# Optimization experiments

Hardware: AMD Instinct MI355X
Metric: run time of the kernel (lower is better)

The kernel has to match this reference:

```python
import jax, jax.numpy as jnp
import numpy as np

EPS = 1e-5

def _bn(x, g, b, axes):
    m = jnp.mean(x, axes, keepdims=True)
    v = jnp.var(x, axes, keepdims=True)
    return (x - m) * jax.lax.rsqrt(v + EPS) * g + b

def _fps(p, m):
    # farthest point sampling: p [B,N,3] -> int32 indices [B,m]
    B, N, _ = p.shape
    def step(carry, _):
        mind, last = carry
        lastp = jnp.take_along_axis(p, last[:, None, None], axis=1)[:, 0]  # [B,3]
        d = jnp.sum((p - lastp[:, None, :]) ** 2, axis=-1)                 # [B,N]
        mind = jnp.minimum(mind, d)
        nxt = jnp.argmax(mind, axis=1).astype(jnp.int32)
        return (mind, nxt), last
    init = (jnp.full((B, N), jnp.inf, p.dtype), jnp.zeros((B,), jnp.int32))
    _, idxs = jax.lax.scan(step, init, None, length=m)  # [m,B]
    return idxs.T

def _gather(x, idx):
    # x [B,N,C], idx [B,...] -> [B,...,C]
    B, C = x.shape[0], x.shape[-1]
    flat = idx.reshape(B, -1)
    out = jnp.take_along_axis(x, flat[:, :, None], axis=1)
    return out.reshape(idx.shape + (C,))

def _transition_down(p, h, W, g, b, stride, nsample):
    # p [B,N,3], h [B,N,C] -> new_p [B,N//stride,3], y [B,N//stride,Cout]
    B, N, _ = p.shape
    M = N // stride
    idx = _fps(p, M)
    new_p = _gather(p, idx)                                               # [B,M,3]
    d = jnp.sum((new_p[:, :, None, :] - p[:, None, :, :]) ** 2, axis=-1)  # [B,M,N]
    _, nidx = jax.lax.top_k(-d, nsample)                                  # [B,M,k]
    gp = _gather(p, nidx) - new_p[:, :, None, :]                          # rel xyz [B,M,k,3]
    gx = _gather(h, nidx)                                                 # [B,M,k,C]
    feat = jnp.concatenate([gp, gx], axis=-1)                             # with_xyz=True
    y = jnp.einsum('bmkc,cd->bmkd', feat, W)
    y = jax.nn.relu(_bn(y, g, b, (0, 1, 2)))
    return new_p, jnp.max(y, axis=2)                                      # MaxPool1d(nsample)

def _forward(x, W1, g1, b1, W2, g2, b2, W3, g3, b3, W4, g4, b4, W5, g5, b5,
             Wc1, bc1, gc1, hc1, Wc2, bc2, gc2, hc2, Wc3, bc3):
    p = x[..., :3]                                    # in_channels == 3 -> features = xyz
    h = jnp.einsum('bnc,cd->bnd', p, W1)
    h = jax.nn.relu(_bn(h, g1, b1, (0, 1)))           # enc1: stride=1
    p, h = _transition_down(p, h, W2, g2, b2, 4, 16)  # enc2
    p, h = _transition_down(p, h, W3, g3, b3, 4, 16)  # enc3
    p, h = _transition_down(p, h, W4, g4, b4, 4, 16)  # enc4
    p, h = _transition_down(p, h, W5, g5, b5, 4, 16)  # enc5
    z = jnp.mean(h, axis=1)                           # segment-mean pool -> [B,512]
    z = jax.nn.relu(_bn(z @ Wc1 + bc1, gc1, hc1, (0,)))   # Dropout = identity (eval)
    z = jax.nn.relu(_bn(z @ Wc2 + bc2, gc2, hc2, (0,)))
    return z @ Wc3 + bc3                              # [B,40]

def setup_inputs() -> dict:
    key = jax.random.key(0)
    ks = jax.random.split(key, 16)
    B, N = 16, 4096
    def lin(k, fi, fo):
        return (jax.random.normal(k, (fi, fo), jnp.float32) / np.sqrt(fi)).astype(jnp.float32)
    inp = {"x": jax.random.normal(ks[0], (B, N, 3), jnp.float32)}
    planes = [32, 64, 128, 256, 512]
    ins = [3, 3 + 32, 3 + 64, 3 + 128, 3 + 256]
    for i, (fi, fo) in enumerate(zip(ins, planes), start=1):
        inp[f"W{i}"] = lin(ks[i], fi, fo)
        inp[f"g{i}"] = jnp.ones((fo,), jnp.float32)
        inp[f"b{i}"] = jnp.zeros((fo,), jnp.float32)
    dims = [(512, 256), (256, 128), (128, 40)]
    for j, (fi, fo) in enumerate(dims, start=1):
        inp[f"Wc{j}"] = lin(ks[5 + j], fi, fo)
        inp[f"bc{j}"] = jnp.zeros((fo,), jnp.float32)
        if j < 3:
            inp[f"gc{j}"] = jnp.ones((fo,), jnp.float32)
            inp[f"hc{j}"] = jnp.zeros((fo,), jnp.float32)
    return inp

def reference(x, W1, g1, b1, W2, g2, b2, W3, g3, b3, W4, g4, b4, W5, g5, b5,
              Wc1, bc1, gc1, hc1, Wc2, bc2, gc2, hc2, Wc3, bc3):
    return _forward(x, W1, g1, b1, W2, g2, b2, W3, g3, b3, W4, g4, b4, W5, g5, b5,
                    Wc1, bc1, gc1, hc1, Wc2, bc2, gc2, hc2, Wc3, bc3)
```

## Files before the change

kernel.cpp:

```cpp
#include <hip/hip_runtime.h>
#include <math.h>
#include <float.h>

#define BN_EPS 1e-5f

__device__ __forceinline__ float sqdist_exact(float dx, float dy, float dz) {
  return __fadd_rn(__fadd_rn(__fmul_rn(dx, dx), __fmul_rn(dy, dy)), __fmul_rn(dz, dz));
}

__global__ void __launch_bounds__(256) mlp1_kernel(const float* __restrict__ x,
                                                   const float* __restrict__ W1,
                                                   float* __restrict__ h1, int rows) {
  int tid = blockIdx.x * 256 + threadIdx.x;
  int row = tid >> 5;
  int d = tid & 31;
  if (row >= rows) return;
  float x0 = x[row * 3 + 0], x1 = x[row * 3 + 1], x2 = x[row * 3 + 2];
  float acc = x0 * W1[d] + x1 * W1[32 + d] + x2 * W1[64 + d];
  h1[row * 32 + d] = acc;
}

__global__ void stats_kernel(const float* __restrict__ v, int n, int D,
                             float* __restrict__ partial) {
  int tid = blockIdx.x * blockDim.x + threadIdx.x;
  int stride = blockDim.x * gridDim.x;
  float s = 0.f, q = 0.f;
  for (int i = tid; i < n; i += stride) { float a = v[i]; s += a; q += a * a; }
  int c = tid % D;
  extern __shared__ float sm[];
  for (int i = threadIdx.x; i < 2 * D; i += blockDim.x) sm[i] = 0.f;
  __syncthreads();
  atomicAdd(&sm[c], s);
  atomicAdd(&sm[D + c], q);
  __syncthreads();
  for (int i = threadIdx.x; i < 2 * D; i += blockDim.x)
    atomicAdd(&partial[(blockIdx.x & 63) * 2 * D + i], sm[i]);
}

__global__ void finalize_kernel(const float* __restrict__ partial,
                                const float* __restrict__ g, const float* __restrict__ b,
                                float cnt, int D, float* __restrict__ ss) {
  int d = threadIdx.x;
  if (d >= D) return;
  float s = 0.f, q = 0.f;
  for (int j = 0; j < 64; j++) { s += partial[j * 2 * D + d]; q += partial[j * 2 * D + D + d]; }
  float mean = s / cnt;
  float var = q / cnt - mean * mean;
  var = fmaxf(var, 0.f);
  float sc = g[d] * rsqrtf(var + BN_EPS);
  ss[d] = sc;
  ss[D + d] = b[d] - mean * sc;
}

__global__ void bn_apply_kernel(float* __restrict__ vmax, const float* __restrict__ vmin,
                                const float* __restrict__ ss, int D, int n) {
  int tid = blockIdx.x * blockDim.x + threadIdx.x;
  int stride = blockDim.x * gridDim.x;
  for (int i = tid; i < n; i += stride) {
    int d = i % D;
    float sc = ss[d], sh = ss[D + d];
    float v = (sc >= 0.f) ? vmax[i] : vmin[i];
    vmax[i] = fmaxf(v * sc + sh, 0.f);
  }
}

#define DPP_STEP(CTRL)                                                                   \
  {                                                                                      \
    unsigned int nhi = (unsigned int)__builtin_amdgcn_update_dpp((int)khi, (int)khi,     \
                                                                 CTRL, 0xf, 0xf, false); \
    unsigned int nlo = (unsigned int)__builtin_amdgcn_update_dpp((int)klo, (int)klo,     \
                                                                 CTRL, 0xf, 0xf, false); \
    unsigned long long nk = (((unsigned long long)nhi) << 32) | nlo;                     \
    if (nk > wk) { wk = nk; khi = nhi; klo = nlo; }                                      \
  }

template <int P, int NW>
__device__ __forceinline__ void fps_body(const float* __restrict__ pb,
                                         float* __restrict__ newp_b,
                                         float* spts, float* snew,
                                         unsigned long long* slots, int t) {
  constexpr int BS = NW * 64;
  constexpr int N = P * BS;
  constexpr int M = N / 4;
  const int wv = t >> 6;
  const int lane = t & 63;
  float px[P], py[P], pz[P], md[P];
#pragma unroll
  for (int j = 0; j < P; j++) {
    int i = j * BS + t;
    float x = pb[3 * i], y = pb[3 * i + 1], z = pb[3 * i + 2];
    px[j] = x; py[j] = y; pz[j] = z; md[j] = INFINITY;
    spts[3 * i] = x; spts[3 * i + 1] = y; spts[3 * i + 2] = z;
  }
  float lx = pb[0], ly = pb[1], lz = pb[2];
  if (t == 0) {
    if constexpr (NW > 1) {
      snew[0] = lx; snew[1] = ly; snew[2] = lz;
    } else {
      newp_b[0] = lx; newp_b[1] = ly; newp_b[2] = lz;
    }
  }

  for (int r = 1; r < M; r++) {
    float bv; int bi;
    {
      float d0 = sqdist_exact(px[0] - lx, py[0] - ly, pz[0] - lz);
      float m0 = fminf(md[0], d0);
      md[0] = m0;
      bv = m0; bi = t;
    }
#pragma unroll
    for (int j = 1; j < P; j++) {
      float d = sqdist_exact(px[j] - lx, py[j] - ly, pz[j] - lz);
      float m = fminf(md[j], d);
      md[j] = m;
      if (m > bv) { bv = m; bi = j * BS + t; }
    }
    unsigned int khi = __float_as_uint(bv);
    unsigned int klo = ~(unsigned int)bi;
    unsigned long long wk = (((unsigned long long)khi) << 32) | klo;
    DPP_STEP(0x111);
    DPP_STEP(0x112);
    DPP_STEP(0x114);
    DPP_STEP(0x118);
    DPP_STEP(0x142);
    DPP_STEP(0x143);
    unsigned int gidx;
    if constexpr (NW == 1) {
      unsigned int wlo = (unsigned int)__builtin_amdgcn_readlane((int)wk, 63);
      gidx = ~wlo;
    } else {
      unsigned long long* base = slots + (r & 1) * NW;
      if (lane == 63) base[wv] = wk;
      __syncthreads();
      unsigned long long fk = base[0];
#pragma unroll
      for (int w = 1; w < NW; w++) {
        unsigned long long k2 = base[w];
        if (k2 > fk) fk = k2;
      }
      gidx = ~(unsigned int)fk;
    }
    lx = spts[3 * gidx];
    ly = spts[3 * gidx + 1];
    lz = spts[3 * gidx + 2];
    if (t == 0) {
      if constexpr (NW > 1) {
        snew[3 * r] = lx; snew[3 * r + 1] = ly; snew[3 * r + 2] = lz;
      } else {
        newp_b[3 * r] = lx; newp_b[3 * r + 1] = ly; newp_b[3 * r + 2] = lz;
      }
    }
  }
  if constexpr (NW > 1) {
    __syncthreads();
    for (int i = t; i < M * 3; i += BS) newp_b[i] = snew[i];
  }
}

template <int P, int NW>
__global__ void __launch_bounds__(NW * 64) fps4_kernel(const float* __restrict__ p,
                                                       float* __restrict__ newp) {
  constexpr int BS = NW * 64;
  constexpr int N = P * BS;
  constexpr int M = N / 4;
  __shared__ float spts[N * 3];
  __shared__ float snew[NW > 1 ? M * 3 : 1];
  __shared__ unsigned long long slots[NW > 1 ? 2 * NW : 2];
  fps_body<P, NW>(p + (size_t)blockIdx.x * N * 3, newp + (size_t)blockIdx.x * M * 3,
                  spts, snew, slots, threadIdx.x);
}

__device__ __forceinline__ void knn_body(const float* __restrict__ p,
                                         const float* __restrict__ newp,
                                         int N, int M, int BM,
                                         int* __restrict__ nidx,
                                         int gwid, int lane) {
  if (gwid >= BM) return;
  int b = gwid / M;
  const float* pb = p + (size_t)b * N * 3;
  float qx = newp[(size_t)gwid * 3], qy = newp[(size_t)gwid * 3 + 1], qz = newp[(size_t)gwid * 3 + 2];
  float bd[16];
  int bi[16];
#pragma unroll
  for (int s = 0; s < 16; s++) { bd[s] = INFINITY; bi[s] = 0x7FFFFFFF; }
  for (int c = lane; c < N; c += 64) {
    float d = sqdist_exact(pb[3 * c] - qx, pb[3 * c + 1] - qy, pb[3 * c + 2] - qz);
    if (d < bd[15]) {
      bd[15] = d; bi[15] = c;
#pragma unroll
      for (int s = 15; s >= 1; --s) {
        bool sw = bd[s] < bd[s - 1];
        if (sw) {
          float tf = bd[s]; bd[s] = bd[s - 1]; bd[s - 1] = tf;
          int ti = bi[s]; bi[s] = bi[s - 1]; bi[s - 1] = ti;
        }
      }
    }
  }
  int out = 0;
  for (int r = 0; r < 16; r++) {
    float v = bd[0]; int ii = bi[0];
    float mv = v; int mi = ii;
#pragma unroll
    for (int m = 1; m < 64; m <<= 1) {
      float v2 = __shfl_xor(mv, m);
      int i2 = __shfl_xor(mi, m);
      if (v2 < mv || (v2 == mv && i2 < mi)) { mv = v2; mi = i2; }
    }
    if (mi == ii) {
#pragma unroll
      for (int s = 0; s < 15; s++) { bd[s] = bd[s + 1]; bi[s] = bi[s + 1]; }
      bd[15] = INFINITY; bi[15] = 0x7FFFFFFF;
    }
    if (lane == r) out = mi;
  }
  if (lane < 16) nidx[(size_t)gwid * 16 + lane] = out;
}

__device__ __forceinline__ void gemm_body(
    float* sm, const float* __restrict__ p, const float* __restrict__ h,
    const float* __restrict__ newp, const int* __restrict__ nidx,
    const float* __restrict__ W, float* __restrict__ ymax, float* __restrict__ ymin,
    float* __restrict__ partial, int N, int M, int BM, int Ch, int Cpad, int D,
    int Gseq, int bid, int t) {
  int Ctot = Ch + 3;
  int TD = D < 256 ? D : 256;
  int Gpar = 256 / TD;
  float* sfeat = sm;
  float* sstat = sm + Gpar * 16 * Cpad;
  for (int i = t; i < 2 * D; i += 256) sstat[i] = 0.f;
  int mloc = t / TD;
  int dbase = t % TD;
  int DV = D / TD;
  __syncthreads();
  for (int s = 0; s < Gseq; s++) {
    int grp0 = (bid * Gseq + s) * Gpar;
    if (grp0 >= BM) break;
    int nf = Gpar * 16 * Cpad;
    for (int i = t; i < nf; i += 256) {
      int c = i % Cpad;
      int rk = i / Cpad;
      int k = rk & 15;
      int g = rk >> 4;
      int grp = grp0 + g;
      float val = 0.f;
      if (grp < BM && c < Ctot) {
        int b = grp / M;
        int nb = nidx[(size_t)grp * 16 + k];
        if (c < 3)
          val = p[((size_t)b * N + nb) * 3 + c] - newp[(size_t)grp * 3 + c];
        else
          val = h[((size_t)b * N + nb) * Ch + (c - 3)];
      }
      sfeat[i] = val;
    }
    __syncthreads();
    int grp = grp0 + mloc;
    bool act = grp < BM;
    const float* fr = sfeat + mloc * 16 * Cpad;
    for (int dv = 0; dv < DV; ++dv) {
      int d = dbase + (dv << 8);
      float acc[16];
#pragma unroll
      for (int k = 0; k < 16; k++) acc[k] = 0.f;
      for (int c = 0; c < Cpad; c += 4) {
        float w0 = (c < Ctot) ? W[(size_t)c * D + d] : 0.f;
        float w1 = (c + 1 < Ctot) ? W[(size_t)(c + 1) * D + d] : 0.f;
        float w2 = (c + 2 < Ctot) ? W[(size_t)(c + 2) * D + d] : 0.f;
        float w3 = (c + 3 < Ctot) ? W[(size_t)(c + 3) * D + d] : 0.f;
#pragma unroll
        for (int k = 0; k < 16; k++) {
          const float4 f = *reinterpret_cast<const float4*>(fr + k * Cpad + c);
          acc[k] += f.x * w0 + f.y * w1 + f.z * w2 + f.w * w3;
        }
      }
      if (act) {
        float ssum = 0.f, ssq = 0.f, amax = -INFINITY, amin = INFINITY;
#pragma unroll
        for (int k = 0; k < 16; k++) {
          float a = acc[k];
          ssum += a; ssq += a * a;
          amax = fmaxf(amax, a); amin = fminf(amin, a);
        }
        ymax[(size_t)grp * D + d] = amax;
        ymin[(size_t)grp * D + d] = amin;
        atomicAdd(&sstat[d], ssum);
        atomicAdd(&sstat[D + d], ssq);
      }
    }
    __syncthreads();
  }
  for (int i = t; i < 2 * D; i += 256)
    atomicAdd(&partial[(bid & 63) * 2 * D + i], sstat[i]);
}

template <int P, int NW>
__global__ void __launch_bounds__(256) fused_fps_knn_kernel(
    const float* __restrict__ fp, float* __restrict__ fnewp,
    const float* __restrict__ kp, const float* __restrict__ knewp,
    int kN, int kM, int kBM, int* __restrict__ knidx) {
  constexpr int BS = NW * 64;
  constexpr int N = P * BS;
  constexpr int M = N / 4;
  __shared__ float spts[N * 3];
  __shared__ float snew[NW > 1 ? M * 3 : 1];
  __shared__ unsigned long long slots[NW > 1 ? 2 * NW : 2];
  const int t = threadIdx.x;
  if (blockIdx.x < 16) {
    if (NW > 1 || t < 64) {
      fps_body<P, NW>(fp + (size_t)blockIdx.x * N * 3, fnewp + (size_t)blockIdx.x * M * 3,
                      spts, snew, slots, t);
    }
  } else {
    int gwid = ((blockIdx.x - 16) * 256 + t) >> 6;
    int lane = t & 63;
    knn_body(kp, knewp, kN, kM, kBM, knidx, gwid, lane);
  }
}

template <int P, int NW>
__global__ void __launch_bounds__(256) fused_gfk_kernel(
    const float* __restrict__ p, const float* __restrict__ h,
    const float* __restrict__ newp, const int* __restrict__ nidx,
    const float* __restrict__ W, float* __restrict__ ymax, float* __restrict__ ymin,
    float* __restrict__ partial, int N, int M, int BM, int Ch, int Cpad, int D,
    int Gseq, int nGemm,
    const float* __restrict__ fp, float* __restrict__ fnewp, int nFps,
    const float* __restrict__ kp, const float* __restrict__ knewp,
    int kN, int kM, int kBM, int* __restrict__ knidx) {
  constexpr int FBS = NW * 64;
  constexpr int FN = P * FBS;
  constexpr int FM = FN / 4;
  __shared__ float spts[FN * 3];
  __shared__ float snew[NW > 1 ? FM * 3 : 1];
  __shared__ unsigned long long slots[NW > 1 ? 2 * NW : 2];
  extern __shared__ float sm[];
  const int t = threadIdx.x;
  const int bid = blockIdx.x;
  if (bid < nGemm) {
    gemm_body(sm, p, h, newp, nidx, W, ymax, ymin, partial,
              N, M, BM, Ch, Cpad, D, Gseq, bid, t);
  } else if (bid < nGemm + nFps) {
    int fb = bid - nGemm;
    if (NW > 1 || t < 64) {
      fps_body<P, NW>(fp + (size_t)fb * FN * 3, fnewp + (size_t)fb * FM * 3,
                      spts, snew, slots, t);
    }
  } else {
    int gwid = ((bid - nGemm - nFps) * 256 + t) >> 6;
    knn_body(kp, knewp, kN, kM, kBM, knidx, gwid, t & 63);
  }
}

__global__ void __launch_bounds__(256) gemm_kernel(
    const float* __restrict__ p, const float* __restrict__ h, const float* __restrict__ newp,
    const int* __restrict__ nidx, const float* __restrict__ W,
    float* __restrict__ ymax, float* __restrict__ ymin, float* __restrict__ partial,
    int N, int M, int BM, int Ch, int Cpad, int D, int Gseq) {
  extern __shared__ float sm[];
  gemm_body(sm, p, h, newp, nidx, W, ymax, ymin, partial,
            N, M, BM, Ch, Cpad, D, Gseq, blockIdx.x, threadIdx.x);
}

__global__ void __launch_bounds__(512) classifier_kernel(
    const float* __restrict__ h4,
    const float* __restrict__ Wc1, const float* __restrict__ bc1,
    const float* __restrict__ gc1, const float* __restrict__ hc1,
    const float* __restrict__ Wc2, const float* __restrict__ bc2,
    const float* __restrict__ gc2, const float* __restrict__ hc2,
    const float* __restrict__ Wc3, const float* __restrict__ bc3,
    float* __restrict__ out) {
  __shared__ float z[16 * 512];
  __shared__ float z1[16 * 256];
  __shared__ float z2[16 * 128];
  __shared__ float sc[256], sh[256];
  int t = threadIdx.x;
  for (int i = t; i < 16 * 512; i += 512) {
    int b = i >> 9, c = i & 511;
    float s = 0.f;
    for (int k = 0; k < 16; k++) s += h4[((size_t)b * 16 + k) * 512 + c];
    z[i] = s * (1.f / 16.f);
  }
  __syncthreads();
  for (int i = t; i < 16 * 256; i += 512) {
    int b = i >> 8, d = i & 255;
    float a = bc1[d];
    for (int c = 0; c < 512; c++) a += z[(b << 9) + c] * Wc1[c * 256 + d];
    z1[i] = a;
  }
  __syncthreads();
  if (t < 256) {
    float s = 0.f, q = 0.f;
    for (int b = 0; b < 16; b++) { float a = z1[(b << 8) + t]; s += a; q += a * a; }
    float mean = s * (1.f / 16.f);
    float var = fmaxf(q * (1.f / 16.f) - mean * mean, 0.f);
    float scl = gc1[t] * rsqrtf(var + BN_EPS);
    sc[t] = scl; sh[t] = hc1[t] - mean * scl;
  }
  __syncthreads();
  for (int i = t; i < 16 * 256; i += 512) {
    int d = i & 255;
    z1[i] = fmaxf(z1[i] * sc[d] + sh[d], 0.f);
  }
  __syncthreads();
  for (int i = t; i < 16 * 128; i += 512) {
    int b = i >> 7, d = i & 127;
    float a = bc2[d];
    for (int c = 0; c < 256; c++) a += z1[(b << 8) + c] * Wc2[c * 128 + d];
    z2[i] = a;
  }
  __syncthreads();
  if (t < 128) {
    float s = 0.f, q = 0.f;
    for (int b = 0; b < 16; b++) { float a = z2[(b << 7) + t]; s += a; q += a * a; }
    float mean = s * (1.f / 16.f);
    float var = fmaxf(q * (1.f / 16.f) - mean * mean, 0.f);
    float scl = gc2[t] * rsqrtf(var + BN_EPS);
    sc[t] = scl; sh[t] = hc2[t] - mean * scl;
  }
  __syncthreads();
  for (int i = t; i < 16 * 128; i += 512) {
    int d = i & 127;
    z2[i] = fmaxf(z2[i] * sc[d] + sh[d], 0.f);
  }
  __syncthreads();
  for (int i = t; i < 640; i += 512) {
    int b = i / 40, d = i % 40;
    float a = bc3[d];
    for (int c = 0; c < 128; c++) a += z2[(b << 7) + c] * Wc3[c * 40 + d];
    out[i] = a;
  }
}

extern "C" void kernel_launch(void* const* d_in, const int* in_sizes, int n_in,
                              void* d_out, int out_size, void* d_ws, size_t ws_size,
                              hipStream_t stream) {
  (void)in_sizes; (void)n_in; (void)out_size; (void)ws_size;
  const float* x   = (const float*)d_in[0];
  const float* W1  = (const float*)d_in[1];
  const float* g1  = (const float*)d_in[2];
  const float* b1  = (const float*)d_in[3];
  const float* W2  = (const float*)d_in[4];
  const float* g2  = (const float*)d_in[5];
  const float* b2  = (const float*)d_in[6];
  const float* W3  = (const float*)d_in[7];
  const float* g3  = (const float*)d_in[8];
  const float* b3  = (const float*)d_in[9];
  const float* W4  = (const float*)d_in[10];
  const float* g4  = (const float*)d_in[11];
  const float* b4  = (const float*)d_in[12];
  const float* W5  = (const float*)d_in[13];
  const float* g5  = (const float*)d_in[14];
  const float* b5  = (const float*)d_in[15];
  const float* Wc1 = (const float*)d_in[16];
  const float* bc1 = (const float*)d_in[17];
  const float* gc1 = (const float*)d_in[18];
  const float* hc1 = (const float*)d_in[19];
  const float* Wc2 = (const float*)d_in[20];
  const float* bc2 = (const float*)d_in[21];
  const float* gc2 = (const float*)d_in[22];
  const float* hc2 = (const float*)d_in[23];
  const float* Wc3 = (const float*)d_in[24];
  const float* bc3 = (const float*)d_in[25];
  float* out = (float*)d_out;

  float* ws = (float*)d_ws;
  float* HA    = ws;
  float* HB    = HA + 2097152;
  float* YMIN  = HB + 1048576;
  float* NP1   = YMIN + 1048576;
  float* NP2   = NP1 + 49152;
  float* NP3   = NP2 + 12288;
  float* NP4   = NP3 + 3072;
  int*   NIDX1 = (int*)(NP4 + 768);
  int*   NIDX2 = NIDX1 + 262144;
  int*   NIDX3 = NIDX2 + 65536;
  int*   NIDX4 = NIDX3 + 16384;
  float* PART  = (float*)(NIDX4 + 4096);
  float* SS    = PART + 5 * 65536;

  hipMemsetAsync(PART, 0, 5 * 65536 * sizeof(float), stream);

  mlp1_kernel<<<(65536 * 32) / 256, 256, 0, stream>>>(x, W1, HA, 65536);
  stats_kernel<<<256, 256, 2 * 32 * sizeof(float), stream>>>(HA, 65536 * 32, 32, PART);
  finalize_kernel<<<1, 32, 0, stream>>>(PART, g1, b1, 65536.f, 32, SS);
  bn_apply_kernel<<<512, 256, 0, stream>>>(HA, HA, SS, 32, 65536 * 32);

  fps4_kernel<16, 4><<<16, 256, 0, stream>>>(x, NP1);
  fused_fps_knn_kernel<4, 4><<<16 + 4096, 256, 0, stream>>>(
      NP1, NP2, x, NP1, 4096, 1024, 16384, NIDX1);

  fused_gfk_kernel<4, 1><<<512 + 16 + 1024, 256, (4 * 16 * 36 + 2 * 64) * sizeof(float), stream>>>(
      x, HA, NP1, NIDX1, W2, HB, YMIN, PART + 65536, 4096, 1024, 16384, 32, 36, 64, 8, 512,
      NP2, NP3, 16,
      NP1, NP2, 1024, 256, 4096, NIDX2);
  finalize_kernel<<<1, 64, 0, stream>>>(PART + 65536, g2, b2, (float)(16384 * 16), 64, SS + 1024);
  bn_apply_kernel<<<512, 256, 0, stream>>>(HB, YMIN, SS + 1024, 64, 16384 * 64);

  fused_gfk_kernel<1, 1><<<512 + 16 + 256, 256, (2 * 16 * 68 + 2 * 128) * sizeof(float), stream>>>(
      NP1, HB, NP2, NIDX2, W3, HA, YMIN, PART + 2 * 65536, 1024, 256, 4096, 64, 68, 128, 4, 512,
      NP3, NP4, 16,
      NP2, NP3, 256, 64, 1024, NIDX3);
  finalize_kernel<<<1, 128, 0, stream>>>(PART + 2 * 65536, g3, b3, (float)(4096 * 16), 128, SS + 2048);
  bn_apply_kernel<<<512, 256, 0, stream>>>(HA, YMIN, SS + 2048, 128, 4096 * 128);

  fused_gfk_kernel<1, 1><<<512 + 0 + 64, 256, (16 * 132 + 2 * 256) * sizeof(float), stream>>>(
      NP2, HA, NP3, NIDX3, W4, HB, YMIN, PART + 3 * 65536, 256, 64, 1024, 128, 132, 256, 2, 512,
      nullptr, nullptr, 0,
      NP3, NP4, 64, 16, 256, NIDX4);
  finalize_kernel<<<1, 256, 0, stream>>>(PART + 3 * 65536, g4, b4, (float)(1024 * 16), 256, SS + 3072);
  bn_apply_kernel<<<512, 256, 0, stream>>>(HB, YMIN, SS + 3072, 256, 1024 * 256);

  gemm_kernel<<<256, 256, (16 * 260 + 2 * 512) * sizeof(float), stream>>>(
      NP3, HB, NP4, NIDX4, W5, HA, YMIN, PART + 4 * 65536, 64, 16, 256, 256, 260, 512, 1);
  finalize_kernel<<<1, 512, 0, stream>>>(PART + 4 * 65536, g5, b5, (float)(256 * 16), 512, SS + 4096);
  bn_apply_kernel<<<512, 256, 0, stream>>>(HA, YMIN, SS + 4096, 512, 256 * 512);

  classifier_kernel<<<1, 512, 0, stream>>>(HA, Wc1, bc1, gc1, hc1, Wc2, bc2, gc2, hc2, Wc3, bc3, out);
}
```

Baseline: 1.378 ms.

## Merge launches: fuse FPS with MLP1, stats into FPS/KNN, finalize into BN apply

Runs the first farthest-point sampling in the same launch as the layer-1 pointwise MLP, and moves the layer-1 BN statistics into the combined FPS/KNN launch as extra blocks. Each finalize+bn_apply pair becomes a single kernel in which every block recomputes the scale and shift from the partial sums. This cuts roughly a dozen small launches and lets the cheap work overlap the serial FPS blocks. In exchange, each of the 512 blocks repeats the 64-way partial reduction.

```diff
diff --git a/kernel.cpp b/kernel.cpp
--- a/kernel.cpp
+++ b/kernel.cpp
@@ -6,62 +6,6 @@
 
 __device__ __forceinline__ float sqdist_exact(float dx, float dy, float dz) {
   return __fadd_rn(__fadd_rn(__fmul_rn(dx, dx), __fmul_rn(dy, dy)), __fmul_rn(dz, dz));
-}
-
-__global__ void __launch_bounds__(256) mlp1_kernel(const float* __restrict__ x,
-                                                   const float* __restrict__ W1,
-                                                   float* __restrict__ h1, int rows) {
-  int tid = blockIdx.x * 256 + threadIdx.x;
-  int row = tid >> 5;
-  int d = tid & 31;
-  if (row >= rows) return;
-  float x0 = x[row * 3 + 0], x1 = x[row * 3 + 1], x2 = x[row * 3 + 2];
-  float acc = x0 * W1[d] + x1 * W1[32 + d] + x2 * W1[64 + d];
-  h1[row * 32 + d] = acc;
-}
-
-__global__ void stats_kernel(const float* __restrict__ v, int n, int D,
-                             float* __restrict__ partial) {
-  int tid = blockIdx.x * blockDim.x + threadIdx.x;
-  int stride = blockDim.x * gridDim.x;
-  float s = 0.f, q = 0.f;
-  for (int i = tid; i < n; i += stride) { float a = v[i]; s += a; q += a * a; }
-  int c = tid % D;
-  extern __shared__ float sm[];
-  for (int i = threadIdx.x; i < 2 * D; i += blockDim.x) sm[i] = 0.f;
-  __syncthreads();
-  atomicAdd(&sm[c], s);
-  atomicAdd(&sm[D + c], q);
-  __syncthreads();
-  for (int i = threadIdx.x; i < 2 * D; i += blockDim.x)
-    atomicAdd(&partial[(blockIdx.x & 63) * 2 * D + i], sm[i]);
-}
-
-__global__ void finalize_kernel(const float* __restrict__ partial,
-                                const float* __restrict__ g, const float* __restrict__ b,
-                                float cnt, int D, float* __restrict__ ss) {
-  int d = threadIdx.x;
-  if (d >= D) return;
-  float s = 0.f, q = 0.f;
-  for (int j = 0; j < 64; j++) { s += partial[j * 2 * D + d]; q += partial[j * 2 * D + D + d]; }
-  float mean = s / cnt;
-  float var = q / cnt - mean * mean;
-  var = fmaxf(var, 0.f);
-  float sc = g[d] * rsqrtf(var + BN_EPS);
-  ss[d] = sc;
-  ss[D + d] = b[d] - mean * sc;
-}
-
-__global__ void bn_apply_kernel(float* __restrict__ vmax, const float* __restrict__ vmin,
-                                const float* __restrict__ ss, int D, int n) {
-  int tid = blockIdx.x * blockDim.x + threadIdx.x;
-  int stride = blockDim.x * gridDim.x;
-  for (int i = tid; i < n; i += stride) {
-    int d = i % D;
-    float sc = ss[d], sh = ss[D + d];
-    float v = (sc >= 0.f) ? vmax[i] : vmin[i];
-    vmax[i] = fmaxf(v * sc + sh, 0.f);
-  }
 }
 
 #define DPP_STEP(CTRL)                                                                   \
@@ -158,19 +102,6 @@
   }
 }
 
-template <int P, int NW>
-__global__ void __launch_bounds__(NW * 64) fps4_kernel(const float* __restrict__ p,
-                                                       float* __restrict__ newp) {
-  constexpr int BS = NW * 64;
-  constexpr int N = P * BS;
-  constexpr int M = N / 4;
-  __shared__ float spts[N * 3];
-  __shared__ float snew[NW > 1 ? M * 3 : 1];
-  __shared__ unsigned long long slots[NW > 1 ? 2 * NW : 2];
-  fps_body<P, NW>(p + (size_t)blockIdx.x * N * 3, newp + (size_t)blockIdx.x * M * 3,
-                  spts, snew, slots, threadIdx.x);
-}
-
 __device__ __forceinline__ void knn_body(const float* __restrict__ p,
                                          const float* __restrict__ newp,
                                          int N, int M, int BM,
@@ -216,6 +147,23 @@
     if (lane == r) out = mi;
   }
   if (lane < 16) nidx[(size_t)gwid * 16 + lane] = out;
+}
+
+__device__ __forceinline__ void stats_body(const float* __restrict__ v, int n, int D,
+                                           float* __restrict__ partial, float* sm,
+                                           int bid, int nb, int t) {
+  int tid = bid * 256 + t;
+  int stride = 256 * nb;
+  float s = 0.f, q = 0.f;
+  for (int i = tid; i < n; i += stride) { float a = v[i]; s += a; q += a * a; }
+  int c = tid % D;
+  for (int i = t; i < 2 * D; i += 256) sm[i] = 0.f;
+  __syncthreads();
+  atomicAdd(&sm[c], s);
+  atomicAdd(&sm[D + c], q);
+  __syncthreads();
+  for (int i = t; i < 2 * D; i += 256)
+    atomicAdd(&partial[(bid & 63) * 2 * D + i], sm[i]);
 }
 
 __device__ __forceinline__ void gemm_body(
@@ -295,27 +243,46 @@
     atomicAdd(&partial[(bid & 63) * 2 * D + i], sstat[i]);
 }
 
-template <int P, int NW>
-__global__ void __launch_bounds__(256) fused_fps_knn_kernel(
+__global__ void __launch_bounds__(256) fused_fps1_mlp1_kernel(
+    const float* __restrict__ x, float* __restrict__ newp,
+    const float* __restrict__ W1, float* __restrict__ h1, int rows) {
+  __shared__ float spts[4096 * 3];
+  __shared__ float snew[1024 * 3];
+  __shared__ unsigned long long slots[8];
+  const int t = threadIdx.x;
+  if (blockIdx.x < 16) {
+    fps_body<16, 4>(x + (size_t)blockIdx.x * 4096 * 3, newp + (size_t)blockIdx.x * 1024 * 3,
+                    spts, snew, slots, t);
+  } else {
+    int tid = (blockIdx.x - 16) * 256 + t;
+    int row = tid >> 5;
+    int d = tid & 31;
+    if (row < rows) {
+      float x0 = x[row * 3 + 0], x1 = x[row * 3 + 1], x2 = x[row * 3 + 2];
+      h1[row * 32 + d] = x0 * W1[d] + x1 * W1[32 + d] + x2 * W1[64 + d];
+    }
+  }
+}
+
+__global__ void __launch_bounds__(256) fused_fks_kernel(
     const float* __restrict__ fp, float* __restrict__ fnewp,
     const float* __restrict__ kp, const float* __restrict__ knewp,
-    int kN, int kM, int kBM, int* __restrict__ knidx) {
-  constexpr int BS = NW * 64;
-  constexpr int N = P * BS;
-  constexpr int M = N / 4;
-  __shared__ float spts[N * 3];
-  __shared__ float snew[NW > 1 ? M * 3 : 1];
-  __shared__ unsigned long long slots[NW > 1 ? 2 * NW : 2];
+    int kN, int kM, int kBM, int* __restrict__ knidx, int nKnn,
+    const float* __restrict__ sv, int sn, int sD, float* __restrict__ spartial, int nStats) {
+  __shared__ float spts[1024 * 3];
+  __shared__ float snew[256 * 3];
+  __shared__ unsigned long long slots[8];
+  __shared__ float ssm[64];
   const int t = threadIdx.x;
-  if (blockIdx.x < 16) {
-    if (NW > 1 || t < 64) {
-      fps_body<P, NW>(fp + (size_t)blockIdx.x * N * 3, fnewp + (size_t)blockIdx.x * M * 3,
-                      spts, snew, slots, t);
-    }
+  const int bid = blockIdx.x;
+  if (bid < 16) {
+    fps_body<4, 4>(fp + (size_t)bid * 1024 * 3, fnewp + (size_t)bid * 256 * 3,
+                   spts, snew, slots, t);
+  } else if (bid < 16 + nKnn) {
+    int gwid = ((bid - 16) * 256 + t) >> 6;
+    knn_body(kp, knewp, kN, kM, kBM, knidx, gwid, t & 63);
   } else {
-    int gwid = ((blockIdx.x - 16) * 256 + t) >> 6;
-    int lane = t & 63;
-    knn_body(kp, knewp, kN, kM, kBM, knidx, gwid, lane);
+    stats_body(sv, sn, sD, spartial, ssm, bid - 16 - nKnn, nStats, t);
   }
 }
 
@@ -361,6 +328,32 @@
   extern __shared__ float sm[];
   gemm_body(sm, p, h, newp, nidx, W, ymax, ymin, partial,
             N, M, BM, Ch, Cpad, D, Gseq, blockIdx.x, threadIdx.x);
+}
+
+__global__ void __launch_bounds__(256) bn_fused_kernel(
+    const float* __restrict__ partial, const float* __restrict__ g,
+    const float* __restrict__ b, float cnt, int D,
+    float* __restrict__ vmax, const float* __restrict__ vmin, int n) {
+  extern __shared__ float ss[];
+  int t = threadIdx.x;
+  for (int d = t; d < D; d += 256) {
+    float s = 0.f, q = 0.f;
+    for (int j = 0; j < 64; j++) { s += partial[j * 2 * D + d]; q += partial[j * 2 * D + D + d]; }
+    float mean = s / cnt;
+    float var = fmaxf(q / cnt - mean * mean, 0.f);
+    float sc = g[d] * rsqrtf(var + BN_EPS);
+    ss[d] = sc;
+    ss[D + d] = b[d] - mean * sc;
+  }
+  __syncthreads();
+  int tid = blockIdx.x * 256 + t;
+  int stride = 256 * gridDim.x;
+  for (int i = tid; i < n; i += stride) {
+    int d = i % D;
+    float sc = ss[d], sh = ss[D + d];
+    float v = (sc >= 0.f) ? vmax[i] : vmin[i];
+    vmax[i] = fmaxf(v * sc + sh, 0.f);
+  }
 }
 
 __global__ void __launch_bounds__(512) classifier_kernel(
@@ -478,44 +471,42 @@
   int*   NIDX3 = NIDX2 + 65536;
   int*   NIDX4 = NIDX3 + 16384;
   float* PART  = (float*)(NIDX4 + 4096);
-  float* SS    = PART + 5 * 65536;
 
   hipMemsetAsync(PART, 0, 5 * 65536 * sizeof(float), stream);
 
-  mlp1_kernel<<<(65536 * 32) / 256, 256, 0, stream>>>(x, W1, HA, 65536);
-  stats_kernel<<<256, 256, 2 * 32 * sizeof(float), stream>>>(HA, 65536 * 32, 32, PART);
-  finalize_kernel<<<1, 32, 0, stream>>>(PART, g1, b1, 65536.f, 32, SS);
-  bn_apply_kernel<<<512, 256, 0, stream>>>(HA, HA, SS, 32, 65536 * 32);
-
-  fps4_kernel<16, 4><<<16, 256, 0, stream>>>(x, NP1);
-  fused_fps_knn_kernel<4, 4><<<16 + 4096, 256, 0, stream>>>(
-      NP1, NP2, x, NP1, 4096, 1024, 16384, NIDX1);
+  fused_fps1_mlp1_kernel<<<16 + 8192, 256, 0, stream>>>(x, NP1, W1, HA, 65536);
+
+  fused_fks_kernel<<<16 + 4096 + 256, 256, 0, stream>>>(
+      NP1, NP2, x, NP1, 4096, 1024, 16384, NIDX1, 4096,
+      HA, 65536 * 32, 32, PART, 256);
+  bn_fused_kernel<<<512, 256, 2 * 32 * sizeof(float), stream>>>(
+      PART, g1, b1, 65536.f, 32, HA, HA, 65536 * 32);
 
   fused_gfk_kernel<4, 1><<<512 + 16 + 1024, 256, (4 * 16 * 36 + 2 * 64) * sizeof(float), stream>>>(
       x, HA, NP1, NIDX1, W2, HB, YMIN, PART + 65536, 4096, 1024, 16384, 32, 36, 64, 8, 512,
       NP2, NP3, 16,
       NP1, NP2, 1024, 256, 4096, NIDX2);
-  finalize_kernel<<<1, 64, 0, stream>>>(PART + 65536, g2, b2, (float)(16384 * 16), 64, SS + 1024);
-  bn_apply_kernel<<<512, 256, 0, stream>>>(HB, YMIN, SS + 1024, 64, 16384 * 64);
+  bn_fused_kernel<<<512, 256, 2 * 64 * sizeof(float), stream>>>(
+      PART + 65536, g2, b2, (float)(16384 * 16), 64, HB, YMIN, 16384 * 64);
 
   fused_gfk_kernel<1, 1><<<512 + 16 + 256, 256, (2 * 16 * 68 + 2 * 128) * sizeof(float), stream>>>(
       NP1, HB, NP2, NIDX2, W3, HA, YMIN, PART + 2 * 65536, 1024, 256, 4096, 64, 68, 128, 4, 512,
       NP3, NP4, 16,
       NP2, NP3, 256, 64, 1024, NIDX3);
-  finalize_kernel<<<1, 128, 0, stream>>>(PART + 2 * 65536, g3, b3, (float)(4096 * 16), 128, SS + 2048);
-  bn_apply_kernel<<<512, 256, 0, stream>>>(HA, YMIN, SS + 2048, 128, 4096 * 128);
+  bn_fused_kernel<<<512, 256, 2 * 128 * sizeof(float), stream>>>(
+      PART + 2 * 65536, g3, b3, (float)(4096 * 16), 128, HA, YMIN, 4096 * 128);
 
   fused_gfk_kernel<1, 1><<<512 + 0 + 64, 256, (16 * 132 + 2 * 256) * sizeof(float), stream>>>(
       NP2, HA, NP3, NIDX3, W4, HB, YMIN, PART + 3 * 65536, 256, 64, 1024, 128, 132, 256, 2, 512,
       nullptr, nullptr, 0,
       NP3, NP4, 64, 16, 256, NIDX4);
-  finalize_kernel<<<1, 256, 0, stream>>>(PART + 3 * 65536, g4, b4, (float)(1024 * 16), 256, SS + 3072);
-  bn_apply_kernel<<<512, 256, 0, stream>>>(HB, YMIN, SS + 3072, 256, 1024 * 256);
+  bn_fused_kernel<<<256, 256, 2 * 256 * sizeof(float), stream>>>(
+      PART + 3 * 65536, g4, b4, (float)(1024 * 16), 256, HB, YMIN, 1024 * 256);
 
   gemm_kernel<<<256, 256, (16 * 260 + 2 * 512) * sizeof(float), stream>>>(
       NP3, HB, NP4, NIDX4, W5, HA, YMIN, PART + 4 * 65536, 64, 16, 256, 256, 260, 512, 1);
-  finalize_kernel<<<1, 512, 0, stream>>>(PART + 4 * 65536, g5, b5, (float)(256 * 16), 512, SS + 4096);
-  bn_apply_kernel<<<512, 256, 0, stream>>>(HA, YMIN, SS + 4096, 512, 256 * 512);
+  bn_fused_kernel<<<64, 256, 2 * 512 * sizeof(float), stream>>>(
+      PART + 4 * 65536, g5, b5, (float)(256 * 16), 512, HA, YMIN, 256 * 512);
 
   classifier_kernel<<<1, 512, 0, stream>>>(HA, Wc1, bc1, gc1, hc1, Wc2, bc2, gc2, hc2, Wc3, bc3, out);
 }
```

New measurement: 1.338 ms. -2.9%, faster.
